# Kernel tuning notes

Hardware: AMD Instinct MI355X
Metric: run time of the kernel (lower is better)

Reference implementation:

```python
import jax, jax.numpy as jnp
import numpy as np

# Static module configuration (matches init_kwargs)
B, CIN, COUT, K, H, W = 4, 32, 32, 3, 128, 128
UM = 2                      # um_dim: 2D vector fields
NW = ((K - 1) // 2) * 4     # num_weights = radius*4 = 4


def setup_inputs() -> dict:
    key = jax.random.key(0)
    k1, k2, k3 = jax.random.split(key, 3)
    params = jax.random.normal(k1, (COUT, CIN, NW, 4), jnp.float32)
    basis = jax.random.normal(k2, (NW, 4, K, K, UM, UM), jnp.float32)
    # Replicate the init-time scaling of the torch module:
    # std over the (non-zero) outer-product kernel, then scale params and basis.
    init_kernel = jnp.einsum('abcd,cdefgh->abcdefgh', params, basis)
    stds = jnp.std(init_kernel)  # random basis -> all entries nonzero
    scaler = jnp.sqrt(0.6 / (np.sqrt(CIN) * (K ** 2) * stds))
    params = params * scaler
    basis = basis * scaler
    bias_term = jnp.ones((1, COUT, 2, 1, 1), jnp.float32) / 100.0
    b = jnp.float32(0.01)
    xx = jax.random.normal(k3, (B, CIN * UM, H, W), jnp.float32)
    return {'xx': xx, 'params': params, 'basis': basis,
            'bias_term': bias_term, 'b': b}


def _forward(xx, params, basis, bias_term, b):
    Bn, C, Hh, Ww = xx.shape
    I, O = CIN, COUT
    # --- get_kernel: einsum + transposes -> conv weight (O*2, I*2, K, K) ---
    Kr = jnp.einsum('abcd,cdefgh->abefgh', params, basis)      # (O,I,K,K,2,2)
    kernel = jnp.transpose(Kr, (0, 4, 1, 5, 2, 3)).reshape(O * 2, I * 2, K, K)
    # --- unfold with replicate padding: P[b,c,kh,kw,h,w] ---
    xp = jnp.pad(xx, ((0, 0), (0, 0), (1, 1), (1, 1)), mode='edge')
    P = jnp.stack([xp[:, :, i:i + Hh, j:j + Ww]
                   for i in range(K) for j in range(K)], axis=2)
    P = P.reshape(Bn, C, K, K, Hh, Ww)
    # --- per-window mean subtraction over (input_channels, kh, kw) ---
    P5 = P.reshape(Bn, I, UM, K, K, Hh, Ww)
    avgs = P5.mean(axis=(1, 3, 4), keepdims=True)              # (B,1,2,1,1,H,W)
    P = (P5 - avgs).reshape(Bn, C, K, K, Hh, Ww)
    avgs = avgs[:, :, :, 0, 0]                                 # (B,1,2,H,W)
    # --- strided conv2d on the blown-up grid == this einsum:
    # big[b,c,3h+di,3w+dj] = P[b,c,kh=dj,kw=di,h,w], so kernel (di,dj)=(p,q)
    # pairs with patch (kh=q, kw=p).
    out = jnp.einsum('bcqphw,ocpq->bohw', P, kernel)           # (B,O*2,H,W)
    out = out.reshape(Bn, O, 2, Hh, Ww) + bias_term
    # --- 'relu' vector activation: normalize, zero where norm <= b ---
    norm = jnp.sqrt(out[:, :, 0] ** 2 + out[:, :, 1] ** 2)[:, :, None]
    out = jnp.where(norm - b <= 0.0, 0.0, out / norm)
    # --- add_mean ---
    out = out + avgs
    return out.reshape(Bn, O * 2, Hh, Ww)


def reference(xx, params, basis, bias_term, b):
    return _forward(xx, params, basis, bias_term, b)
```

## Files before the change

kernel.cpp:

```cpp
#include <hip/hip_runtime.h>

#define BN 4
#define CH 64
#define HH 128
#define WW 128
#define PIX (HH*WW)

#define OFF_WL  0
#define OFF_S   36864
#define OFF_AVG 36992

#define SR 24
#define SCH (18*SR)
#define NCELL 324
#define NSTAGE (8*NCELL)

__device__ __forceinline__ int iclamp(int v, int lo, int hi) {
    return v < lo ? lo : (v > hi ? hi : v);
}

__global__ __launch_bounds__(256) void k_prep(const float* __restrict__ params,
                                              const float* __restrict__ basis,
                                              const float* __restrict__ x,
                                              float* __restrict__ Wl,
                                              float* __restrict__ S,
                                              float* __restrict__ avg) {
    int bx = blockIdx.x;
    if (bx < 144) {
        int idx = bx * 256 + threadIdx.x;
        int oc  = idx & 63;
        int tap = (idx >> 6) % 9;
        int c   = idx / 576;
        int q = tap / 3, p = tap % 3;
        int o = oc >> 1, g = oc & 1;
        int i = c >> 1, u = c & 1;
        float s = 0.f;
        #pragma unroll
        for (int n = 0; n < 4; ++n)
            #pragma unroll
            for (int d = 0; d < 4; ++d)
                s = fmaf(params[((o * 32 + i) * 4 + n) * 4 + d],
                         basis[((((n * 4 + d) * 3 + p) * 3 + q) * 2 + g) * 2 + u], s);
        Wl[(((oc >> 4) * 64 + c) * 9 + tap) * 16 + (oc & 15)] = s;
    } else if (bx == 144) {
        int t = threadIdx.x;
        if (t < 128) {
            int u = t >> 6, oc = t & 63;
            int o = oc >> 1, g = oc & 1;
            float s = 0.f;
            #pragma unroll
            for (int nd = 0; nd < 16; ++nd) {
                int n = nd >> 2, d = nd & 3;
                float pa = 0.f;
                for (int i = 0; i < 32; ++i)
                    pa += params[((o * 32 + i) * 4 + n) * 4 + d];
                float sb = 0.f;
                #pragma unroll
                for (int e = 0; e < 3; ++e)
                    #pragma unroll
                    for (int f = 0; f < 3; ++f)
                        sb += basis[((((n * 4 + d) * 3 + e) * 3 + f) * 2 + g) * 2 + u];
                s = fmaf(pa, sb, s);
            }
            S[t] = s;
        }
    } else {
        int id = bx - 145;
        int tile = id & 63;
        int u    = (id >> 6) & 1;
        int b    = id >> 7;
        int ty0 = (tile >> 3) * 16, tx0 = (tile & 7) * 16;

        __shared__ float hs[18][19];
        int t = threadIdx.x;
        for (int cell = t; cell < 324; cell += 256) {
            int hy = cell / 18, hx = cell - (cell / 18) * 18;
            int gy = iclamp(ty0 + hy - 1, 0, HH - 1);
            int gx = iclamp(tx0 + hx - 1, 0, WW - 1);
            const float* xp = x + ((size_t)b * CH + u) * PIX + gy * WW + gx;
            float s = 0.f;
            #pragma unroll
            for (int i = 0; i < 32; ++i) s += xp[(size_t)i * 2 * PIX];
            hs[hy][hx] = s;
        }
        __syncthreads();
        int py = t >> 4, px = t & 15;
        float s = hs[py][px]     + hs[py][px + 1]     + hs[py][px + 2]
                + hs[py + 1][px] + hs[py + 1][px + 1] + hs[py + 1][px + 2]
                + hs[py + 2][px] + hs[py + 2][px + 1] + hs[py + 2][px + 2];
        avg[(size_t)(b * 2 + u) * PIX + (ty0 + py) * WW + (tx0 + px)] = s * (1.0f / 288.0f);
    }
}

__global__ __launch_bounds__(256, 4) void k_main(
    const float* __restrict__ x,
    const float* __restrict__ Wl,
    const float* __restrict__ S,
    const float* __restrict__ bias,
    const float* __restrict__ avg,
    const float* __restrict__ bptr,
    float* __restrict__ out)
{
    __shared__ float sm[8 * SCH];

    int tile = blockIdx.x;
    int ocg  = blockIdx.y;
    int b    = blockIdx.z;
    int ty = threadIdx.x >> 4, tx = threadIdx.x & 15;
    int h0 = (tile >> 3) * 16, w0 = (tile & 7) * 16;
    int h = h0 + ty, w = w0 + tx;

    const float* xb = x + (size_t)b * CH * PIX;

    int goff[11], loff[11];
    #pragma unroll
    for (int k = 0; k < 11; ++k) {
        int cell = threadIdx.x + (k << 8);
        if (cell >= NSTAGE) cell = NSTAGE - 1;
        int cc = cell / NCELL;
        int r  = cell - cc * NCELL;
        int hy = r / 18, hx = r - (r / 18) * 18;
        int gy = iclamp(h0 - 1 + hy, 0, HH - 1);
        int gx = iclamp(w0 - 1 + hx, 0, WW - 1);
        goff[k] = cc * PIX + gy * WW + gx;
        loff[k] = cc * SCH + hy * SR + hx;
    }
    bool act10 = threadIdx.x < (NSTAGE - 2560);
    int lrd = ty * SR + tx;

    float acc[16];
    #pragma unroll
    for (int j = 0; j < 16; ++j) acc[j] = 0.f;

    {
        #pragma unroll
        for (int k = 0; k < 10; ++k) sm[loff[k]] = xb[goff[k]];
        if (act10) sm[loff[10]] = xb[goff[10]];
    }
    __syncthreads();

    const float* wbase = Wl + (size_t)ocg * 64 * 144;

    for (int c0 = 0; c0 < CH; c0 += 8) {
        float xf[11];
        bool more = (c0 + 8 < CH);
        if (more) {
            const float* xn = xb + (size_t)(c0 + 8) * PIX;
            #pragma unroll
            for (int k = 0; k < 10; ++k) xf[k] = xn[goff[k]];
            if (act10) xf[10] = xn[goff[10]];
        }

        const float* wc = wbase + c0 * 144;
        #pragma unroll
        for (int cc = 0; cc < 8; ++cc) {
            float xv[9];
            #pragma unroll
            for (int dy = 0; dy < 3; ++dy)
                #pragma unroll
                for (int dx = 0; dx < 3; ++dx)
                    xv[dy * 3 + dx] = sm[lrd + cc * SCH + dy * SR + dx];
            const float* wt = wc + cc * 144;
            #pragma unroll
            for (int t = 0; t < 9; ++t) {
                float xt = xv[t];
                #pragma unroll
                for (int j = 0; j < 16; ++j)
                    acc[j] = fmaf(xt, wt[t * 16 + j], acc[j]);
            }
        }

        if (more) {
            __syncthreads();
            #pragma unroll
            for (int k = 0; k < 10; ++k) sm[loff[k]] = xf[k];
            if (act10) sm[loff[10]] = xf[10];
            __syncthreads();
        }
    }

    int pix = h * WW + w;
    float a0 = avg[(size_t)(b * 2 + 0) * PIX + pix];
    float a1 = avg[(size_t)(b * 2 + 1) * PIX + pix];
    float bthr = bptr[0];

    float* ob = out + (size_t)b * CH * PIX + pix;
    #pragma unroll
    for (int j = 0; j < 16; j += 2) {
        int oc = ocg * 16 + j;
        float t0 = acc[j]     - a0 * S[oc]     - a1 * S[64 + oc]     + bias[oc];
        float t1 = acc[j + 1] - a0 * S[oc + 1] - a1 * S[64 + oc + 1] + bias[oc + 1];
        float n = sqrtf(t0 * t0 + t1 * t1);
        float r0, r1;
        if (n - bthr <= 0.f) { r0 = 0.f; r1 = 0.f; }
        else { r0 = t0 / n; r1 = t1 / n; }
        ob[(size_t)oc * PIX]       = r0 + a0;
        ob[(size_t)(oc + 1) * PIX] = r1 + a1;
    }
}

extern "C" void kernel_launch(void* const* d_in, const int* in_sizes, int n_in,
                              void* d_out, int out_size, void* d_ws, size_t ws_size,
                              hipStream_t stream) {
    const float* xx     = (const float*)d_in[0];
    const float* params = (const float*)d_in[1];
    const float* basis  = (const float*)d_in[2];
    const float* bias   = (const float*)d_in[3];
    const float* bptr   = (const float*)d_in[4];
    float* out = (float*)d_out;
    float* ws  = (float*)d_ws;

    float* Wl  = ws + OFF_WL;
    float* S   = ws + OFF_S;
    float* avg = ws + OFF_AVG;

    k_prep<<<657, 256, 0, stream>>>(params, basis, xx, Wl, S, avg);

    dim3 grid(64, 4, BN);
    k_main<<<grid, 256, 0, stream>>>(xx, Wl, S, bias, avg, bptr, out);
}
```

Measured before the change: 138.4 us.

## Shrink main tiles to 8x8 and move window-mean 3x3 sum into epilogue

The main conv kernel now uses 64-thread blocks over 8x8 pixel tiles, which gives a 4x larger grid (4096 blocks) and more parallelism for the 256 CUs. The prep kernel now only produces per-pixel channel sums with vectorized float4 loads. The 3x3 box sum for the window mean moves into the main kernel epilogue. The cost is a larger halo overhead: 10x10 staged cells per 64 pixels instead of 18x18 per 256. Each block also repeats the weight loads, and the epilogue does 18 extra global reads per pixel.

```diff
diff --git a/kernel.cpp b/kernel.cpp
--- a/kernel.cpp
+++ b/kernel.cpp
@@ -8,11 +8,11 @@
 
 #define OFF_WL  0
 #define OFF_S   36864
-#define OFF_AVG 36992
-
-#define SR 24
-#define SCH (18*SR)
-#define NCELL 324
+#define OFF_CS  36992
+
+#define SR 12
+#define SCH (10*SR)
+#define NCELL 100
 #define NSTAGE (8*NCELL)
 
 __device__ __forceinline__ int iclamp(int v, int lo, int hi) {
@@ -24,7 +24,7 @@
                                               const float* __restrict__ x,
                                               float* __restrict__ Wl,
                                               float* __restrict__ S,
-                                              float* __restrict__ avg) {
+                                              float* __restrict__ cs) {
     int bx = blockIdx.x;
     if (bx < 144) {
         int idx = bx * 256 + threadIdx.x;
@@ -65,39 +65,27 @@
             S[t] = s;
         }
     } else {
-        int id = bx - 145;
-        int tile = id & 63;
-        int u    = (id >> 6) & 1;
-        int b    = id >> 7;
-        int ty0 = (tile >> 3) * 16, tx0 = (tile & 7) * 16;
-
-        __shared__ float hs[18][19];
-        int t = threadIdx.x;
-        for (int cell = t; cell < 324; cell += 256) {
-            int hy = cell / 18, hx = cell - (cell / 18) * 18;
-            int gy = iclamp(ty0 + hy - 1, 0, HH - 1);
-            int gx = iclamp(tx0 + hx - 1, 0, WW - 1);
-            const float* xp = x + ((size_t)b * CH + u) * PIX + gy * WW + gx;
-            float s = 0.f;
-            #pragma unroll
-            for (int i = 0; i < 32; ++i) s += xp[(size_t)i * 2 * PIX];
-            hs[hy][hx] = s;
-        }
-        __syncthreads();
-        int py = t >> 4, px = t & 15;
-        float s = hs[py][px]     + hs[py][px + 1]     + hs[py][px + 2]
-                + hs[py + 1][px] + hs[py + 1][px + 1] + hs[py + 1][px + 2]
-                + hs[py + 2][px] + hs[py + 2][px + 1] + hs[py + 2][px + 2];
-        avg[(size_t)(b * 2 + u) * PIX + (ty0 + py) * WW + (tx0 + px)] = s * (1.0f / 288.0f);
-    }
-}
-
-__global__ __launch_bounds__(256, 4) void k_main(
+        int idx = (bx - 145) * 256 + threadIdx.x;
+        int pq  = idx & (PIX / 4 - 1);
+        int u   = (idx >> 12) & 1;
+        int b   = idx >> 13;
+        const float4* xb = (const float4*)x;
+        float4 s = make_float4(0.f, 0.f, 0.f, 0.f);
+        #pragma unroll
+        for (int i = 0; i < 32; ++i) {
+            float4 v = xb[(size_t)(b * CH + 2 * i + u) * (PIX / 4) + pq];
+            s.x += v.x; s.y += v.y; s.z += v.z; s.w += v.w;
+        }
+        ((float4*)cs)[(b * 2 + u) * (PIX / 4) + pq] = s;
+    }
+}
+
+__global__ __launch_bounds__(64, 4) void k_main(
     const float* __restrict__ x,
     const float* __restrict__ Wl,
     const float* __restrict__ S,
     const float* __restrict__ bias,
-    const float* __restrict__ avg,
+    const float* __restrict__ cs,
     const float* __restrict__ bptr,
     float* __restrict__ out)
 {
@@ -106,49 +94,48 @@
     int tile = blockIdx.x;
     int ocg  = blockIdx.y;
     int b    = blockIdx.z;
-    int ty = threadIdx.x >> 4, tx = threadIdx.x & 15;
-    int h0 = (tile >> 3) * 16, w0 = (tile & 7) * 16;
-    int h = h0 + ty, w = w0 + tx;
+    int tid = threadIdx.x;
+    int py = tid >> 3, px = tid & 7;
+    int h0 = (tile >> 4) * 8, w0 = (tile & 15) * 8;
+    int h = h0 + py, w = w0 + px;
 
     const float* xb = x + (size_t)b * CH * PIX;
 
-    int goff[11], loff[11];
-    #pragma unroll
-    for (int k = 0; k < 11; ++k) {
-        int cell = threadIdx.x + (k << 8);
+    int goff[13], loff[13];
+    #pragma unroll
+    for (int k = 0; k < 13; ++k) {
+        int cell = tid + (k << 6);
         if (cell >= NSTAGE) cell = NSTAGE - 1;
         int cc = cell / NCELL;
         int r  = cell - cc * NCELL;
-        int hy = r / 18, hx = r - (r / 18) * 18;
+        int hy = r / 10, hx = r - (r / 10) * 10;
         int gy = iclamp(h0 - 1 + hy, 0, HH - 1);
         int gx = iclamp(w0 - 1 + hx, 0, WW - 1);
         goff[k] = cc * PIX + gy * WW + gx;
         loff[k] = cc * SCH + hy * SR + hx;
     }
-    bool act10 = threadIdx.x < (NSTAGE - 2560);
-    int lrd = ty * SR + tx;
+    bool act12 = tid < (NSTAGE - 768);
+    int lrd = py * SR + px;
 
     float acc[16];
     #pragma unroll
     for (int j = 0; j < 16; ++j) acc[j] = 0.f;
 
-    {
-        #pragma unroll
-        for (int k = 0; k < 10; ++k) sm[loff[k]] = xb[goff[k]];
-        if (act10) sm[loff[10]] = xb[goff[10]];
-    }
+    #pragma unroll
+    for (int k = 0; k < 12; ++k) sm[loff[k]] = xb[goff[k]];
+    if (act12) sm[loff[12]] = xb[goff[12]];
     __syncthreads();
 
     const float* wbase = Wl + (size_t)ocg * 64 * 144;
 
     for (int c0 = 0; c0 < CH; c0 += 8) {
-        float xf[11];
+        float xf[13];
         bool more = (c0 + 8 < CH);
         if (more) {
             const float* xn = xb + (size_t)(c0 + 8) * PIX;
             #pragma unroll
-            for (int k = 0; k < 10; ++k) xf[k] = xn[goff[k]];
-            if (act10) xf[10] = xn[goff[10]];
+            for (int k = 0; k < 12; ++k) xf[k] = xn[goff[k]];
+            if (act12) xf[12] = xn[goff[12]];
         }
 
         const float* wc = wbase + c0 * 144;
@@ -173,15 +160,24 @@
         if (more) {
             __syncthreads();
             #pragma unroll
-            for (int k = 0; k < 10; ++k) sm[loff[k]] = xf[k];
-            if (act10) sm[loff[10]] = xf[10];
+            for (int k = 0; k < 12; ++k) sm[loff[k]] = xf[k];
+            if (act12) sm[loff[12]] = xf[12];
             __syncthreads();
         }
     }
 
     int pix = h * WW + w;
-    float a0 = avg[(size_t)(b * 2 + 0) * PIX + pix];
-    float a1 = avg[(size_t)(b * 2 + 1) * PIX + pix];
+    int hm = h > 0 ? h - 1 : 0, hp = h < HH - 1 ? h + 1 : HH - 1;
+    int wm = w > 0 ? w - 1 : 0, wp = w < WW - 1 ? w + 1 : WW - 1;
+    const float* c0p = cs + (size_t)(b * 2 + 0) * PIX;
+    const float* c1p = cs + (size_t)(b * 2 + 1) * PIX;
+    int r0 = hm * WW, r1 = h * WW, r2 = hp * WW;
+    float a0 = (c0p[r0 + wm] + c0p[r0 + w] + c0p[r0 + wp]
+              + c0p[r1 + wm] + c0p[r1 + w] + c0p[r1 + wp]
+              + c0p[r2 + wm] + c0p[r2 + w] + c0p[r2 + wp]) * (1.0f / 288.0f);
+    float a1 = (c1p[r0 + wm] + c1p[r0 + w] + c1p[r0 + wp]
+              + c1p[r1 + wm] + c1p[r1 + w] + c1p[r1 + wp]
+              + c1p[r2 + wm] + c1p[r2 + w] + c1p[r2 + wp]) * (1.0f / 288.0f);
     float bthr = bptr[0];
 
     float* ob = out + (size_t)b * CH * PIX + pix;
@@ -191,11 +187,11 @@
         float t0 = acc[j]     - a0 * S[oc]     - a1 * S[64 + oc]     + bias[oc];
         float t1 = acc[j + 1] - a0 * S[oc + 1] - a1 * S[64 + oc + 1] + bias[oc + 1];
         float n = sqrtf(t0 * t0 + t1 * t1);
-        float r0, r1;
-        if (n - bthr <= 0.f) { r0 = 0.f; r1 = 0.f; }
-        else { r0 = t0 / n; r1 = t1 / n; }
-        ob[(size_t)oc * PIX]       = r0 + a0;
-        ob[(size_t)(oc + 1) * PIX] = r1 + a1;
+        float r0v, r1v;
+        if (n - bthr <= 0.f) { r0v = 0.f; r1v = 0.f; }
+        else { r0v = t0 / n; r1v = t1 / n; }
+        ob[(size_t)oc * PIX]       = r0v + a0;
+        ob[(size_t)(oc + 1) * PIX] = r1v + a1;
     }
 }
 
@@ -212,10 +208,10 @@
 
     float* Wl  = ws + OFF_WL;
     float* S   = ws + OFF_S;
-    float* avg = ws + OFF_AVG;
-
-    k_prep<<<657, 256, 0, stream>>>(params, basis, xx, Wl, S, avg);
-
-    dim3 grid(64, 4, BN);
-    k_main<<<grid, 256, 0, stream>>>(xx, Wl, S, bias, avg, bptr, out);
-}
+    float* cs  = ws + OFF_CS;
+
+    k_prep<<<273, 256, 0, stream>>>(params, basis, xx, Wl, S, cs);
+
+    dim3 grid(256, 4, BN);
+    k_main<<<grid, 64, 0, stream>>>(xx, Wl, S, bias, cs, bptr, out);
+}
```

After: 147.0 us. 1.06x slower.
